# Performance work log

Measured on AMD Instinct MI355X. Metric: run time of the kernel, lower is better.

## Reference

```python
import jax, jax.numpy as jnp
import numpy as np

D_MODEL = 1024
N_HEADS = 16
HEAD_DIM = D_MODEL // N_HEADS
EPS = 1e-6


def _phi(x):
    # elu(x) + 1 feature map
    return jax.nn.elu(x) + 1.0


def setup_inputs() -> dict:
    key = jax.random.key(0)
    ks = jax.random.split(key, 12)
    B, N, M = 4, 4096, 4096
    s = 1.0 / np.sqrt(D_MODEL)
    return {
        "queries": jax.random.normal(ks[0], (B, N, D_MODEL), jnp.float32),
        "keys": jax.random.normal(ks[1], (B, M, D_MODEL), jnp.float32),
        "values": jax.random.normal(ks[2], (B, M, D_MODEL), jnp.float32),
        "wq": jax.random.normal(ks[3], (D_MODEL, D_MODEL), jnp.float32) * s,
        "bq": jax.random.normal(ks[4], (D_MODEL,), jnp.float32) * s,
        "wk": jax.random.normal(ks[5], (D_MODEL, D_MODEL), jnp.float32) * s,
        "bk": jax.random.normal(ks[6], (D_MODEL,), jnp.float32) * s,
        "wv": jax.random.normal(ks[7], (D_MODEL, D_MODEL), jnp.float32) * s,
        "bv": jax.random.normal(ks[8], (D_MODEL,), jnp.float32) * s,
        "wo": jax.random.normal(ks[9], (D_MODEL, D_MODEL), jnp.float32) * s,
        "bo": jax.random.normal(ks[10], (D_MODEL,), jnp.float32) * s,
    }


def reference(queries, keys, values, wq, bq, wk, bk, wv, bv, wo, bo):
    B, N, _ = queries.shape
    M = keys.shape[1]
    H, Dh = N_HEADS, HEAD_DIM
    # projections + head split -> [B, H, seq, Dh]
    q = _phi((queries @ wq.T + bq).reshape(B, N, H, Dh).transpose(0, 2, 1, 3))
    k = _phi((keys @ wk.T + bk).reshape(B, M, H, Dh).transpose(0, 2, 1, 3))
    v = (values @ wv.T + bv).reshape(B, M, H, Dh).transpose(0, 2, 1, 3)
    # kv aggregation: [B,H,Dh,Dh]
    kv = jnp.einsum("bhmd,bhme->bhde", k, v)
    # normalizer: [B,H,Dh]
    z = k.sum(axis=2)
    num = jnp.einsum("bhnd,bhde->bhne", q, kv)
    den = jnp.einsum("bhnd,bhd->bhn", q, z)[..., None] + EPS
    out = (num / den).transpose(0, 2, 1, 3).reshape(B, N, H * Dh)
    return out @ wo.T + bo
```

## Files before the change

### kernel.cpp

```cpp
#include <hip/hip_runtime.h>

#define EPS 1e-6f

typedef __attribute__((ext_vector_type(8))) __bf16 bf16x8;
typedef __attribute__((ext_vector_type(4))) float f32x4;
typedef __attribute__((ext_vector_type(4))) unsigned short us4v;
typedef __attribute__((ext_vector_type(8))) unsigned short us8v;
typedef unsigned short us;

__device__ inline us f2bf(float f) {
  unsigned int u = __builtin_bit_cast(unsigned int, f);
  unsigned int r = (u + 0x7fffu + ((u >> 16) & 1u)) >> 16;
  return (us)r;
}
__device__ inline float bf2f(us s) {
  unsigned int u = ((unsigned int)s) << 16;
  return __builtin_bit_cast(float, u);
}

__device__ inline void gl_lds16(const us* g, us* l) {
  __builtin_amdgcn_global_load_lds(
      (const __attribute__((address_space(1))) unsigned int*)g,
      (__attribute__((address_space(3))) unsigned int*)l, 16, 0, 0);
}

__global__ __launch_bounds__(256) void conv_bf16(const float* __restrict__ s,
                                                 us* __restrict__ d) {
  int idx = blockIdx.x * 256 + threadIdx.x;
  size_t base = (size_t)idx * 8;
  float4 a = *(const float4*)(s + base);
  float4 b = *(const float4*)(s + base + 4);
  us8v o;
  o[0] = f2bf(a.x); o[1] = f2bf(a.y); o[2] = f2bf(a.z); o[3] = f2bf(a.w);
  o[4] = f2bf(b.x); o[5] = f2bf(b.y); o[6] = f2bf(b.z); o[7] = f2bf(b.w);
  *(us8v*)(d + base) = o;
}

template <int MODE>
__global__ __launch_bounds__(256) void proj_gemm(const us* __restrict__ X,
                                                 const us* __restrict__ W,
                                                 const float* __restrict__ bias,
                                                 void* __restrict__ Yv) {
  __shared__ alignas(16) us Xs[128 * 64];
  __shared__ alignas(16) us Ws[128 * 64];

  const int t = threadIdx.x;
  const int wave = t >> 6, lane = t & 63;
  const int q4 = lane >> 4, l16 = lane & 15;
  const int wm = wave & 1, wn = wave >> 1;
  const int bid = blockIdx.x;
  const int colBase = (bid >> 7) << 7;
  const int rowBase = (bid & 127) << 7;

  const int srow0 = t >> 3;
  const int spos = (t & 7) ^ (srow0 & 7);
  const us* Xg = X + (size_t)rowBase * 1024 + (size_t)srow0 * 1024 + spos * 8;
  const us* Wg = W + (size_t)colBase * 1024 + (size_t)srow0 * 1024 + spos * 8;

  f32x4 acc[4][4];
#pragma unroll
  for (int i = 0; i < 4; i++)
#pragma unroll
    for (int j = 0; j < 4; j++) acc[i][j] = (f32x4){0.f, 0.f, 0.f, 0.f};

  for (int k0 = 0; k0 < 1024; k0 += 64) {
#pragma unroll
    for (int i = 0; i < 4; i++) {
      gl_lds16(Xg + (size_t)i * 32 * 1024 + k0, &Xs[(i * 256 + wave * 64) * 8]);
      gl_lds16(Wg + (size_t)i * 32 * 1024 + k0, &Ws[(i * 256 + wave * 64) * 8]);
    }
    __syncthreads();

#pragma unroll
    for (int ks = 0; ks < 2; ks++) {
      bf16x8 af[4], bfr[4];
#pragma unroll
      for (int i = 0; i < 4; i++) {
        int r = wm * 64 + i * 16 + l16;
        af[i] = *(const bf16x8*)&Xs[r * 64 + ((((ks << 2) | q4)) ^ (r & 7)) * 8];
      }
#pragma unroll
      for (int j = 0; j < 4; j++) {
        int r = wn * 64 + j * 16 + l16;
        bfr[j] = *(const bf16x8*)&Ws[r * 64 + ((((ks << 2) | q4)) ^ (r & 7)) * 8];
      }
#pragma unroll
      for (int i = 0; i < 4; i++)
#pragma unroll
        for (int j = 0; j < 4; j++)
          acc[i][j] = __builtin_amdgcn_mfma_f32_16x16x32_bf16(af[i], bfr[j], acc[i][j], 0, 0, 0);
    }
    __syncthreads();
  }

#pragma unroll
  for (int j = 0; j < 4; j++) {
    int col = colBase + wn * 64 + j * 16 + l16;
    float bv = bias[col];
#pragma unroll
    for (int i = 0; i < 4; i++) {
      int row0 = rowBase + wm * 64 + i * 16 + q4 * 4;
      if (MODE == 1 || MODE == 2) {
        int b = row0 >> 12, m0 = row0 & 4095;
        int h = col >> 6, dd = col & 63;
        us4v pk;
#pragma unroll
        for (int r = 0; r < 4; r++) {
          float y = acc[i][j][r] + bv;
          if (MODE == 1) y = (y > 0.f) ? (y + 1.f) : __expf(y);
          pk[r] = f2bf(y);
        }
        *(us4v*)&((us*)Yv)[(((size_t)((b * 16 + h) * 64 + dd)) << 12) + m0] = pk;
      } else {
#pragma unroll
        for (int r = 0; r < 4; r++) {
          float y = acc[i][j][r] + bv;
          if (MODE == 0) {
            y = (y > 0.f) ? (y + 1.f) : __expf(y);
            ((us*)Yv)[(size_t)(row0 + r) * 1024 + col] = f2bf(y);
          } else {
            ((float*)Yv)[(size_t)(row0 + r) * 1024 + col] = y;
          }
        }
      }
    }
  }
}

__global__ __launch_bounds__(256) void kv_stage1(const us* __restrict__ kt,
                                                 const us* __restrict__ vt,
                                                 float* __restrict__ part,
                                                 float* __restrict__ zpart) {
  __shared__ float red[4][4096];
  __shared__ float zred[4][64][4];

  const int blk = blockIdx.x;
  const int bh = blk >> 2, split = blk & 3;
  const int t = threadIdx.x;
  const int w = t >> 6, lane = t & 63;
  const int q4 = lane >> 4, l16 = lane & 15;
  const us* ktb = kt + (size_t)bh * 64 * 4096;
  const us* vtb = vt + (size_t)bh * 64 * 4096;
  const int mbeg = split * 1024 + w * 256;

  f32x4 acc[4][4];
#pragma unroll
  for (int i = 0; i < 4; i++)
#pragma unroll
    for (int j = 0; j < 4; j++) acc[i][j] = (f32x4){0.f, 0.f, 0.f, 0.f};
  float zacc[4] = {0.f, 0.f, 0.f, 0.f};

  for (int m0 = mbeg; m0 < mbeg + 256; m0 += 32) {
    bf16x8 af[4], bfr[4];
#pragma unroll
    for (int i = 0; i < 4; i++)
      af[i] = *(const bf16x8*)&vtb[(size_t)(i * 16 + l16) * 4096 + m0 + q4 * 8];
#pragma unroll
    for (int j = 0; j < 4; j++) {
      us8v ub = *(const us8v*)&ktb[(size_t)(j * 16 + l16) * 4096 + m0 + q4 * 8];
      bfr[j] = __builtin_bit_cast(bf16x8, ub);
#pragma unroll
      for (int e = 0; e < 8; e++) zacc[j] += bf2f(ub[e]);
    }
#pragma unroll
    for (int i = 0; i < 4; i++)
#pragma unroll
      for (int j = 0; j < 4; j++)
        acc[i][j] = __builtin_amdgcn_mfma_f32_16x16x32_bf16(af[i], bfr[j], acc[i][j], 0, 0, 0);
  }

#pragma unroll
  for (int i = 0; i < 4; i++)
#pragma unroll
    for (int j = 0; j < 4; j++)
#pragma unroll
      for (int r = 0; r < 4; r++)
        red[w][(i * 16 + q4 * 4 + r) * 64 + j * 16 + l16] = acc[i][j][r];
#pragma unroll
  for (int j = 0; j < 4; j++) zred[w][j * 16 + l16][q4] = zacc[j];
  __syncthreads();

  float* pb = part + (size_t)blk * 4096;
#pragma unroll
  for (int i = 0; i < 16; i++) {
    int idx = t + 256 * i;
    pb[idx] = red[0][idx] + red[1][idx] + red[2][idx] + red[3][idx];
  }
  if (t < 64) {
    float s = 0.f;
#pragma unroll
    for (int w2 = 0; w2 < 4; w2++)
#pragma unroll
      for (int q = 0; q < 4; q++) s += zred[w2][t][q];
    zpart[blk * 64 + t] = s;
  }
}

__global__ __launch_bounds__(256) void kv_stage2(const float* __restrict__ part,
                                                 const float* __restrict__ zpart,
                                                 us* __restrict__ kvb,
                                                 float* __restrict__ z) {
  const int bh = blockIdx.x;
  const int t = threadIdx.x;
  const float* p0 = part + (size_t)bh * 4 * 4096;
#pragma unroll
  for (int i = 0; i < 16; i++) {
    int idx = t + 256 * i;
    float s = p0[idx] + p0[4096 + idx] + p0[8192 + idx] + p0[12288 + idx];
    kvb[(size_t)bh * 4096 + idx] = f2bf(s);
  }
  if (t < 64) {
    const float* zp = zpart + (size_t)bh * 4 * 64;
    z[bh * 64 + t] = zp[t] + zp[64 + t] + zp[128 + t] + zp[192 + t];
  }
}

__global__ __launch_bounds__(256) void attn_kernel(const us* __restrict__ q,
                                                   const us* __restrict__ kvb,
                                                   const float* __restrict__ z,
                                                   us* __restrict__ attn) {
  __shared__ alignas(16) us kvs[64 * 72];
  __shared__ float zs[64];
  __shared__ float invden[256];

  const int bid = blockIdx.x;
  const int bh = bid >> 4, nc = bid & 15;
  const int b = bh >> 4, h = bh & 15;
  const int n0 = nc * 256;
  const int t = threadIdx.x;
  const int wave = t >> 6, lane = t & 63;
  const int q4 = lane >> 4, l16 = lane & 15;

#pragma unroll
  for (int i = 0; i < 2; i++) {
    int chunk = t + 256 * i;
    int e = chunk >> 3, d8 = chunk & 7;
    us8v vv = *(const us8v*)&kvb[(size_t)bh * 4096 + chunk * 8];
    *(us8v*)&kvs[e * 72 + d8 * 8] = vv;
  }
  if (t < 64) zs[t] = z[bh * 64 + t];
  __syncthreads();

  {
    const us* qrow = q + ((size_t)(b * 4096 + n0 + t)) * 1024 + h * 64;
    float s = 0.f;
#pragma unroll
    for (int d0 = 0; d0 < 64; d0 += 8) {
      us8v v = *(const us8v*)(qrow + d0);
#pragma unroll
      for (int j = 0; j < 8; j++) s += bf2f(v[j]) * zs[d0 + j];
    }
    invden[t] = 1.0f / (s + EPS);
  }
  __syncthreads();

  f32x4 acc[4][4];
#pragma unroll
  for (int i = 0; i < 4; i++)
#pragma unroll
    for (int j = 0; j < 4; j++) acc[i][j] = (f32x4){0.f, 0.f, 0.f, 0.f};

  const us* qb = q + ((size_t)(b * 4096 + n0 + wave * 64)) * 1024 + h * 64;
#pragma unroll
  for (int ks = 0; ks < 2; ks++) {
    bf16x8 af[4], bfr[4];
#pragma unroll
    for (int i = 0; i < 4; i++)
      af[i] = *(const bf16x8*)(qb + (size_t)(i * 16 + l16) * 1024 + ks * 32 + q4 * 8);
#pragma unroll
    for (int j = 0; j < 4; j++)
      bfr[j] = *(const bf16x8*)&kvs[(j * 16 + l16) * 72 + ks * 32 + q4 * 8];
#pragma unroll
    for (int i = 0; i < 4; i++)
#pragma unroll
      for (int j = 0; j < 4; j++)
        acc[i][j] = __builtin_amdgcn_mfma_f32_16x16x32_bf16(af[i], bfr[j], acc[i][j], 0, 0, 0);
  }

  us* ab = attn + ((size_t)(b * 4096 + n0 + wave * 64)) * 1024 + h * 64;
#pragma unroll
  for (int i = 0; i < 4; i++)
#pragma unroll
    for (int j = 0; j < 4; j++)
#pragma unroll
      for (int r = 0; r < 4; r++) {
        int rowl = i * 16 + q4 * 4 + r;
        int nl = wave * 64 + rowl;
        int e = j * 16 + l16;
        ab[(size_t)rowl * 1024 + e] = f2bf(acc[i][j][r] * invden[nl]);
      }
}

extern "C" void kernel_launch(void* const* d_in, const int* in_sizes, int n_in,
                              void* d_out, int out_size, void* d_ws, size_t ws_size,
                              hipStream_t stream) {
  const float* queries = (const float*)d_in[0];
  const float* keys    = (const float*)d_in[1];
  const float* values  = (const float*)d_in[2];
  const float* wq = (const float*)d_in[3];
  const float* bq = (const float*)d_in[4];
  const float* wk = (const float*)d_in[5];
  const float* bk = (const float*)d_in[6];
  const float* wv = (const float*)d_in[7];
  const float* bv = (const float*)d_in[8];
  const float* wo = (const float*)d_in[9];
  const float* bo = (const float*)d_in[10];

  char* ws = (char*)d_ws;
  const size_t TB = (size_t)16384 * 1024 * 2;
  us* A   = (us*)(ws);
  us* Bb  = (us*)(ws + TB);
  us* Xb  = (us*)(ws + 2 * TB);
  us* wqb = (us*)(ws + 3 * TB);
  us* wkb = wqb + (size_t)1024 * 1024;
  us* wvb = wkb + (size_t)1024 * 1024;
  us* wob = wvb + (size_t)1024 * 1024;
  float* part  = (float*)(wob + (size_t)1024 * 1024);
  float* zpart = part + (size_t)256 * 4096;
  float* z     = zpart + 256 * 64;
  us* kvb      = (us*)(z + 4096);

  const int GRID_IN = 16384 * 1024 / 2048;
  const int GRID_W  = 1024 * 1024 / 2048;

  conv_bf16<<<GRID_W, 256, 0, stream>>>(wq, wqb);
  conv_bf16<<<GRID_W, 256, 0, stream>>>(wk, wkb);
  conv_bf16<<<GRID_W, 256, 0, stream>>>(wv, wvb);
  conv_bf16<<<GRID_W, 256, 0, stream>>>(wo, wob);

  conv_bf16<<<GRID_IN, 256, 0, stream>>>(keys, Xb);
  proj_gemm<1><<<1024, 256, 0, stream>>>(Xb, wkb, bk, (void*)A);
  conv_bf16<<<GRID_IN, 256, 0, stream>>>(values, Xb);
  proj_gemm<2><<<1024, 256, 0, stream>>>(Xb, wvb, bv, (void*)Bb);
  kv_stage1<<<256, 256, 0, stream>>>(A, Bb, part, zpart);
  kv_stage2<<<64, 256, 0, stream>>>(part, zpart, kvb, z);
  conv_bf16<<<GRID_IN, 256, 0, stream>>>(queries, Bb);
  proj_gemm<0><<<1024, 256, 0, stream>>>(Bb, wqb, bq, (void*)A);
  attn_kernel<<<1024, 256, 0, stream>>>(A, kvb, z, A);
  proj_gemm<3><<<1024, 256, 0, stream>>>(A, wob, bo, d_out);
}
```

Baseline: 464.2 us.

## Rewrite projection GEMM with 256x256 tiles and a 4-stage async LDS pipeline

Restructures the bf16 projection GEMM to use 512-thread blocks computing 256x256 output tiles with K-step 32, fed by a 4-deep ring of LDS buffers filled via global_load_lds, with explicit vmcnt waits and raw s_barrier instead of __syncthreads. It also remaps block indices so rows and columns are grouped for L2 reuse and raises MFMA priority with s_setprio. The goal is to hide global load latency behind MFMA work and raise arithmetic intensity per block. The cost is higher register pressure from 32 accumulators per wave, larger LDS use, and only 256 blocks, which on a 256-CU part leaves little room for load balancing.

```diff
diff --git a/kernel.cpp b/kernel.cpp
--- a/kernel.cpp
+++ b/kernel.cpp
@@ -37,69 +37,93 @@
 }
 
 template <int MODE>
-__global__ __launch_bounds__(256) void proj_gemm(const us* __restrict__ X,
-                                                 const us* __restrict__ W,
-                                                 const float* __restrict__ bias,
-                                                 void* __restrict__ Yv) {
-  __shared__ alignas(16) us Xs[128 * 64];
-  __shared__ alignas(16) us Ws[128 * 64];
+__global__ __launch_bounds__(512, 2) void proj_gemm(const us* __restrict__ X,
+                                                    const us* __restrict__ W,
+                                                    const float* __restrict__ bias,
+                                                    void* __restrict__ Yv) {
+  __shared__ alignas(16) us As[4][256 * 32];
+  __shared__ alignas(16) us Bs[4][256 * 32];
 
   const int t = threadIdx.x;
   const int wave = t >> 6, lane = t & 63;
   const int q4 = lane >> 4, l16 = lane & 15;
-  const int wm = wave & 1, wn = wave >> 1;
+  const int wm = wave >> 2, wn = wave & 3;
   const int bid = blockIdx.x;
-  const int colBase = (bid >> 7) << 7;
-  const int rowBase = (bid & 127) << 7;
-
-  const int srow0 = t >> 3;
-  const int spos = (t & 7) ^ (srow0 & 7);
-  const us* Xg = X + (size_t)rowBase * 1024 + (size_t)srow0 * 1024 + spos * 8;
-  const us* Wg = W + (size_t)colBase * 1024 + (size_t)srow0 * 1024 + spos * 8;
-
-  f32x4 acc[4][4];
-#pragma unroll
-  for (int i = 0; i < 4; i++)
+  const int rowg = (bid & 7) * 8 + (bid >> 5);
+  const int colg = (bid >> 3) & 3;
+  const int rowBase = rowg << 8;
+  const int colBase = colg << 8;
+
+  const int spos = (t & 3) ^ ((t >> 3) & 3);
+  const us* Xg = X + (size_t)(rowBase + (t >> 2)) * 1024 + spos * 8;
+  const us* Wg = W + (size_t)(colBase + (t >> 2)) * 1024 + spos * 8;
+  const int cA = (q4 ^ ((l16 >> 1) & 3)) * 8;
+
+  f32x4 acc[8][4];
+#pragma unroll
+  for (int i = 0; i < 8; i++)
 #pragma unroll
     for (int j = 0; j < 4; j++) acc[i][j] = (f32x4){0.f, 0.f, 0.f, 0.f};
 
-  for (int k0 = 0; k0 < 1024; k0 += 64) {
-#pragma unroll
-    for (int i = 0; i < 4; i++) {
-      gl_lds16(Xg + (size_t)i * 32 * 1024 + k0, &Xs[(i * 256 + wave * 64) * 8]);
-      gl_lds16(Wg + (size_t)i * 32 * 1024 + k0, &Ws[(i * 256 + wave * 64) * 8]);
+#define STAGEP(tt)                                                         \
+  {                                                                        \
+    const int k0_ = (tt) * 32;                                             \
+    us* Ad_ = &As[(tt) & 3][wave * 64 * 8];                                \
+    us* Bd_ = &Bs[(tt) & 3][wave * 64 * 8];                                \
+    gl_lds16(Xg + k0_, Ad_);                                               \
+    gl_lds16(Xg + (size_t)128 * 1024 + k0_, Ad_ + 512 * 8);                \
+    gl_lds16(Wg + k0_, Bd_);                                               \
+    gl_lds16(Wg + (size_t)128 * 1024 + k0_, Bd_ + 512 * 8);                \
+  }
+
+  STAGEP(0);
+  STAGEP(1);
+  STAGEP(2);
+
+#pragma unroll 4
+  for (int tt = 0; tt < 32; ++tt) {
+    if (tt < 29) {
+      STAGEP(tt + 3);
+      asm volatile("s_waitcnt vmcnt(12)" ::: "memory");
+    } else if (tt == 29) {
+      asm volatile("s_waitcnt vmcnt(8)" ::: "memory");
+    } else if (tt == 30) {
+      asm volatile("s_waitcnt vmcnt(4)" ::: "memory");
+    } else {
+      asm volatile("s_waitcnt vmcnt(0)" ::: "memory");
     }
-    __syncthreads();
-
-#pragma unroll
-    for (int ks = 0; ks < 2; ks++) {
-      bf16x8 af[4], bfr[4];
-#pragma unroll
-      for (int i = 0; i < 4; i++) {
-        int r = wm * 64 + i * 16 + l16;
-        af[i] = *(const bf16x8*)&Xs[r * 64 + ((((ks << 2) | q4)) ^ (r & 7)) * 8];
-      }
-#pragma unroll
-      for (int j = 0; j < 4; j++) {
-        int r = wn * 64 + j * 16 + l16;
-        bfr[j] = *(const bf16x8*)&Ws[r * 64 + ((((ks << 2) | q4)) ^ (r & 7)) * 8];
-      }
-#pragma unroll
-      for (int i = 0; i < 4; i++)
-#pragma unroll
-        for (int j = 0; j < 4; j++)
-          acc[i][j] = __builtin_amdgcn_mfma_f32_16x16x32_bf16(af[i], bfr[j], acc[i][j], 0, 0, 0);
-    }
-    __syncthreads();
-  }
+    asm volatile("s_barrier" ::: "memory");
+
+    const us* Ab = &As[tt & 3][0];
+    const us* Bb2 = &Bs[tt & 3][0];
+    bf16x8 af[8], bfv[4];
+#pragma unroll
+    for (int i = 0; i < 8; i++)
+      af[i] = *(const bf16x8*)&Ab[(wm * 128 + i * 16 + l16) * 32 + cA];
+#pragma unroll
+    for (int j = 0; j < 4; j++)
+      bfv[j] = *(const bf16x8*)&Bb2[(wn * 64 + j * 16 + l16) * 32 + cA];
+
+    __builtin_amdgcn_s_setprio(1);
+#pragma unroll
+    for (int i = 0; i < 8; i++)
+#pragma unroll
+      for (int j = 0; j < 4; j++)
+        acc[i][j] = __builtin_amdgcn_mfma_f32_16x16x32_bf16(af[i], bfv[j],
+                                                            acc[i][j], 0, 0, 0);
+    __builtin_amdgcn_s_setprio(0);
+
+    asm volatile("s_barrier" ::: "memory");
+  }
+#undef STAGEP
 
 #pragma unroll
   for (int j = 0; j < 4; j++) {
     int col = colBase + wn * 64 + j * 16 + l16;
     float bv = bias[col];
 #pragma unroll
-    for (int i = 0; i < 4; i++) {
-      int row0 = rowBase + wm * 64 + i * 16 + q4 * 4;
+    for (int i = 0; i < 8; i++) {
+      int row0 = rowBase + wm * 128 + i * 16 + q4 * 4;
       if (MODE == 1 || MODE == 2) {
         int b = row0 >> 12, m0 = row0 & 4095;
         int h = col >> 6, dd = col & 63;
@@ -329,13 +353,13 @@
   conv_bf16<<<GRID_W, 256, 0, stream>>>(wo, wob);
 
   conv_bf16<<<GRID_IN, 256, 0, stream>>>(keys, Xb);
-  proj_gemm<1><<<1024, 256, 0, stream>>>(Xb, wkb, bk, (void*)A);
+  proj_gemm<1><<<256, 512, 0, stream>>>(Xb, wkb, bk, (void*)A);
   conv_bf16<<<GRID_IN, 256, 0, stream>>>(values, Xb);
-  proj_gemm<2><<<1024, 256, 0, stream>>>(Xb, wvb, bv, (void*)Bb);
+  proj_gemm<2><<<256, 512, 0, stream>>>(Xb, wvb, bv, (void*)Bb);
   kv_stage1<<<256, 256, 0, stream>>>(A, Bb, part, zpart);
   kv_stage2<<<64, 256, 0, stream>>>(part, zpart, kvb, z);
   conv_bf16<<<GRID_IN, 256, 0, stream>>>(queries, Bb);
-  proj_gemm<0><<<1024, 256, 0, stream>>>(Bb, wqb, bq, (void*)A);
+  proj_gemm<0><<<256, 512, 0, stream>>>(Bb, wqb, bq, (void*)A);
   attn_kernel<<<1024, 256, 0, stream>>>(A, kvb, z, A);
-  proj_gemm<3><<<1024, 256, 0, stream>>>(A, wob, bo, d_out);
-}
+  proj_gemm<3><<<256, 512, 0, stream>>>(A, wob, bo, d_out);
+}
```

New measurement: 440.4 us. -5.1%, faster.
